# Kernel optimization log

Measured on AMD Instinct MI355X. Metric: run time of the kernel, lower is better.

The kernel has to match this reference:

```python
import jax, jax.numpy as jnp
import numpy as np

N = 50000        # nodes
E = 800000       # edges (before self-loops)
IN = 128         # in_dim
H = 2            # heads
C1 = 64          # hidden_dim (per head)
D1 = H * C1      # conv1 concat output = 128
OUT = 64         # out_dim
C2 = 2 * OUT     # conv2 per-head channels = 128 (concat=False -> mean over heads)
NEG = 0.2        # GATv2 leaky_relu negative slope
EPS = 1e-5       # BatchNorm eps


def setup_inputs() -> dict:
    key = jax.random.key(0)
    ks = jax.random.split(key, 14)
    s = 0.05
    inp = {
        "x": jax.random.normal(ks[0], (N, IN), jnp.float32),
        "edge_index": jax.random.randint(ks[1], (2, E), 0, N, dtype=jnp.int32),
        # conv1 (GATv2: lin_l for source, lin_r for target, att vector per head)
        "W_l1": jax.random.normal(ks[2], (IN, D1), jnp.float32) * s,
        "b_l1": jnp.zeros((D1,), jnp.float32),
        "W_r1": jax.random.normal(ks[3], (IN, D1), jnp.float32) * s,
        "b_r1": jnp.zeros((D1,), jnp.float32),
        "att1": jax.random.normal(ks[4], (H, C1), jnp.float32) * s,
        "bias1": jnp.zeros((D1,), jnp.float32),
        # batch_norm1 (affine)
        "gamma1": jnp.ones((D1,), jnp.float32),
        "beta1": jnp.zeros((D1,), jnp.float32),
        # conv2
        "W_l2": jax.random.normal(ks[5], (D1, H * C2), jnp.float32) * s,
        "b_l2": jnp.zeros((H * C2,), jnp.float32),
        "W_r2": jax.random.normal(ks[6], (D1, H * C2), jnp.float32) * s,
        "b_r2": jnp.zeros((H * C2,), jnp.float32),
        "att2": jax.random.normal(ks[7], (H, C2), jnp.float32) * s,
        "bias2": jnp.zeros((C2,), jnp.float32),
    }
    return inp


def gatv2_layer(x, src, dst, W_l, b_l, W_r, b_r, att, bias, concat):
    Hh, Cc = att.shape
    x_l = (x @ W_l + b_l).reshape(N, Hh, Cc)   # source transform
    x_r = (x @ W_r + b_r).reshape(N, Hh, Cc)   # target transform
    # per-edge GATv2 score: att . leaky_relu(x_l[j] + x_r[i])
    e = jax.nn.leaky_relu(x_l[src] + x_r[dst], NEG)      # [E', H, C]
    logit = jnp.einsum("ehc,hc->eh", e, att)              # [E', H]
    # segment softmax over incoming edges of each target node
    m = jax.ops.segment_max(logit, dst, num_segments=N)   # [N, H]
    ex = jnp.exp(logit - m[dst])
    den = jax.ops.segment_sum(ex, dst, num_segments=N)    # [N, H]
    alpha = ex / den[dst]                                  # [E', H]
    out = jax.ops.segment_sum(x_l[src] * alpha[:, :, None], dst, num_segments=N)
    out = out.reshape(N, Hh * Cc) if concat else out.mean(axis=1)
    return out + bias


def batchnorm(x, gamma=None, beta=None):
    mu = x.mean(axis=0)
    var = x.var(axis=0)  # biased variance, as used by BN for normalization
    xn = (x - mu) * jax.lax.rsqrt(var + EPS)
    if gamma is not None:
        xn = xn * gamma + beta
    return xn


def reference(x, edge_index, W_l1, b_l1, W_r1, b_r1, att1, bias1, gamma1, beta1,
              W_l2, b_l2, W_r2, b_r2, att2, bias2):
    loops = jnp.arange(N, dtype=edge_index.dtype)
    src = jnp.concatenate([edge_index[0], loops])  # add self-loops (PyG default)
    dst = jnp.concatenate([edge_index[1], loops])
    h = gatv2_layer(x, src, dst, W_l1, b_l1, W_r1, b_r1, att1, bias1, True)
    h = jax.nn.relu(batchnorm(h, gamma1, beta1))
    o = gatv2_layer(h, src, dst, W_l2, b_l2, W_r2, b_r2, att2, bias2, False)
    mu_part = batchnorm(o[:, :OUT])                      # affine=False
    return jnp.concatenate([mu_part, jax.nn.softplus(o[:, OUT:])], axis=1)
```

## Files before the change

### kernel.cpp

```cpp
#include <hip/hip_runtime.h>
#include <hip/hip_bf16.h>
#include <math.h>

#define NNODES 50000
#define NEDGES 800000
#define EPTOT  (NEDGES + NNODES)
#define NEG_SLOPE 0.2f
#define BN_EPS 1e-5f
#define LOG2E 1.44269504088896f
#define ESLOT 64

#define PB_SC  3321
#define PB_W1  (PB_SC + 128)
#define PB_W2  (PB_W1 + 256)

typedef __hip_bfloat16 bf16;
typedef __attribute__((ext_vector_type(8))) short short8;
typedef __attribute__((ext_vector_type(4))) float f32x4;
typedef __attribute__((ext_vector_type(2))) float f32x2;

__device__ __forceinline__ unsigned short f2us(float f){
    return (unsigned short)(__bfloat16_as_ushort(__float2bfloat16(f)));
}
__device__ __forceinline__ f32x2 unpk(unsigned int w){
    union { unsigned int u; float f; } lo, hi;
    lo.u = w << 16; hi.u = w & 0xffff0000u;
    f32x2 r; r.x = lo.f; r.y = hi.f; return r;
}
__device__ __forceinline__ f32x2 pkmax(f32x2 a, f32x2 b){
#if __has_builtin(__builtin_elementwise_max)
    return __builtin_elementwise_max(a, b);
#else
    f32x2 r; r.x = fmaxf(a.x, b.x); r.y = fmaxf(a.y, b.y); return r;
#endif
}
__device__ __forceinline__ unsigned int pack2(float a, float b){
    return (unsigned int)f2us(a) | ((unsigned int)f2us(b) << 16);
}

template<int CTRL>
__device__ __forceinline__ float dppadd(float v){
    int p = __builtin_amdgcn_update_dpp(0, __float_as_int(v), CTRL, 0xf, 0xf, true);
    return v + __int_as_float(p);
}
template<int G>
__device__ __forceinline__ float group_sum(float v){
    if constexpr (G == 16){
        v = dppadd<0x121>(v);
        v = dppadd<0x122>(v);
        v = dppadd<0x124>(v);
        v = dppadd<0x128>(v);
    } else {
        v = dppadd<0xB1>(v);
        v = dppadd<0x4E>(v);
        v += __shfl_xor(v, 4, 64);
    }
    return v;
}


__global__ __launch_bounds__(256) void misc_prep(
    const int* __restrict__ ei, int* __restrict__ cnt, int* __restrict__ esrc,
    const float* __restrict__ Wl1, const float* __restrict__ Wr1,
    const float* __restrict__ bl1, const float* __restrict__ br1,
    bf16* __restrict__ WT1, float* __restrict__ bc1,
    const float* __restrict__ Wl2, const float* __restrict__ Wr2,
    const float* __restrict__ bl2, const float* __restrict__ br2,
    bf16* __restrict__ WT2, float* __restrict__ bc2)
{
    int b = blockIdx.x;
    if (b < PB_SC){
        int e = b * 256 + threadIdx.x;
        if (e < EPTOT){
            int s, d;
            if (e < NEDGES){ s = ei[e]; d = ei[NEDGES + e]; } else { s = d = e - NEDGES; }
            int pos = atomicAdd(&cnt[d], 1);
            if (pos < ESLOT) esrc[(d << 6) + pos] = s;
        }
    } else if (b < PB_W1){
        int i = (b - PB_SC) * 256 + threadIdx.x;
        int r = i >> 7, k = i & 127;
        const float* W = (r < 128) ? Wl1 : Wr1;
        int c = (r < 128) ? r : r - 128;
        WT1[i] = __float2bfloat16(W[k * 128 + c]);
        if (k == 0) bc1[r] = (r < 128) ? bl1[c] : br1[c];
    } else {
        int i = (b - PB_W1) * 256 + threadIdx.x;
        int r = i >> 7, k = i & 127;
        const float* W = (r < 256) ? Wl2 : Wr2;
        int c = (r < 256) ? r : r - 256;
        WT2[i] = __float2bfloat16(W[k * 256 + c]);
        if (k == 0) bc2[r] = (r < 256) ? bl2[c] : br2[c];
    }
}


template<int DTOT, bool F32A, int NT>
__global__ __launch_bounds__(128) void mfma_gemm(
    const void* __restrict__ A, const bf16* __restrict__ WT,
    const float* __restrict__ biascat,
    bf16* __restrict__ xl, bf16* __restrict__ xr)
{
    int wave = threadIdx.x >> 6;
    int lane = threadIdx.x & 63;
    int quad = lane >> 4;
    int l16  = lane & 15;
    int m0 = blockIdx.x * 128 + wave * 64;
    const short* Ap = (const short*)A;
    const float* Af = (const float*)A;
    const short* Bp = (const short*)WT;

    short8 af[4][4];
    #pragma unroll
    for (int k = 0; k < 4; ++k)
        #pragma unroll
        for (int mt = 0; mt < 4; ++mt){
            int m = m0 + mt * 16 + l16;
            m = (m < NNODES) ? m : (NNODES - 1);
            if (F32A){
                float4 v0 = *(const float4*)(Af + (size_t)m * 128 + k * 32 + quad * 8);
                float4 v1 = *(const float4*)(Af + (size_t)m * 128 + k * 32 + quad * 8 + 4);
                unsigned int* u = (unsigned int*)&af[k][mt];
                u[0] = pack2(v0.x, v0.y); u[1] = pack2(v0.z, v0.w);
                u[2] = pack2(v1.x, v1.y); u[3] = pack2(v1.z, v1.w);
            } else {
                af[k][mt] = *(const short8*)(Ap + (size_t)m * 128 + k * 32 + quad * 8);
            }
        }

    for (int t = 0; t < NT; ++t){
        int n0 = (blockIdx.y * NT + t) * 64;
        f32x4 acc[4][4] = {};
        #pragma unroll
        for (int k = 0; k < 4; ++k){
            short8 bfr[4];
            #pragma unroll
            for (int nt = 0; nt < 4; ++nt){
                int n = n0 + nt * 16 + l16;
                bfr[nt] = *(const short8*)(Bp + (size_t)n * 128 + k * 32 + quad * 8);
            }
            #pragma unroll
            for (int mt = 0; mt < 4; ++mt)
                #pragma unroll
                for (int nt = 0; nt < 4; ++nt)
                    acc[mt][nt] = __builtin_amdgcn_mfma_f32_16x16x32_bf16(af[k][mt], bfr[nt], acc[mt][nt], 0, 0, 0);
        }
        #pragma unroll
        for (int nt = 0; nt < 4; ++nt){
            int n = n0 + nt * 16 + l16;
            float bi = biascat[n];
            bf16* outp = (n < DTOT) ? xl : xr;
            int c = (n < DTOT) ? n : n - DTOT;
            #pragma unroll
            for (int mt = 0; mt < 4; ++mt)
                #pragma unroll
                for (int r = 0; r < 4; ++r){
                    int m = m0 + mt * 16 + quad * 4 + r;
                    if (m < NNODES)
                        outp[(size_t)m * DTOT + c] = __float2bfloat16(acc[mt][nt][r] + bi);
                }
        }
    }
}


template<int C, bool MEAN>
__global__ __launch_bounds__(128) void gat_aggregate(
    const bf16* __restrict__ xl, const bf16* __restrict__ xr,
    const float* __restrict__ att, const int* __restrict__ cnt,
    const int* __restrict__ esrc, void* __restrict__ outv,
    const float* __restrict__ bias2)
{
    constexpr int G  = C / 8;
    constexpr int E  = 64 / G;
    constexpr int HC = 2 * C;
    __shared__ float tmp[HC];
    int n    = blockIdx.x;
    int lane = threadIdx.x & 63;
    int head = threadIdx.x >> 6;
    int g    = lane / G;
    int cl   = lane % G;
    int rowoff = head * (C * 2) + cl * 16;
    const char* xlp = (const char*)xl;

    int srcAll = esrc[(n << 6) + lane];
    int cc = cnt[n];
    int c = (cc < ESLOT) ? cc : ESLOT;
    uint4 xw = *(const uint4*)((const char*)xr + (unsigned)(n * (HC * 2) + rowoff));
    f32x2 xr0 = unpk(xw.x), xr1 = unpk(xw.y), xr2v = unpk(xw.z), xr3 = unpk(xw.w);
    const float* ap = att + head * C + cl * 8;
    f32x2 av0 = {ap[0] * LOG2E, ap[1] * LOG2E};
    f32x2 av1 = {ap[2] * LOG2E, ap[3] * LOG2E};
    f32x2 av2 = {ap[4] * LOG2E, ap[5] * LOG2E};
    f32x2 av3 = {ap[6] * LOG2E, ap[7] * LOG2E};

    float den = 0.f;
    f32x2 a0 = {0.f,0.f}, a1 = {0.f,0.f}, a2 = {0.f,0.f}, a3 = {0.f,0.f};

    int ia0 = g, ib0 = E + g;
    int sa = __shfl(srcAll, (ia0 < c) ? ia0 : (c - 1), 64);
    int sb = __shfl(srcAll, (ib0 < c) ? ib0 : (c - 1), 64);

    int p = 0;
    for (; p + E < c; p += 2 * E){
        uint4 wa = *(const uint4*)(xlp + ((unsigned)sa * (unsigned)(HC * 2) + rowoff));
        uint4 wb = *(const uint4*)(xlp + ((unsigned)sb * (unsigned)(HC * 2) + rowoff));
        float mkb = (p + E + g < c) ? 0.f : -1e30f;

        int pn = p + 2 * E;
        int ian = pn + g, ibn = pn + E + g;
        int sa_n = __shfl(srcAll, (ian < c) ? ian : (c - 1), 64);
        int sb_n = __shfl(srcAll, (ibn < c) ? ibn : (c - 1), 64);

        f32x2 xa0 = unpk(wa.x), xa1 = unpk(wa.y), xa2 = unpk(wa.z), xa3 = unpk(wa.w);
        f32x2 xb0 = unpk(wb.x), xb1 = unpk(wb.y), xb2 = unpk(wb.z), xb3 = unpk(wb.w);

        f32x2 ua0 = xa0 + xr0, ua1 = xa1 + xr1, ua2 = xa2 + xr2v, ua3 = xa3 + xr3;
        f32x2 ub0 = xb0 + xr0, ub1 = xb1 + xr1, ub2 = xb2 + xr2v, ub3 = xb3 + xr3;

        f32x2 ppa = pkmax(ua0, ua0 * NEG_SLOPE) * av0;
        ppa += pkmax(ua1, ua1 * NEG_SLOPE) * av1;
        ppa += pkmax(ua2, ua2 * NEG_SLOPE) * av2;
        ppa += pkmax(ua3, ua3 * NEG_SLOPE) * av3;
        f32x2 ppb = pkmax(ub0, ub0 * NEG_SLOPE) * av0;
        ppb += pkmax(ub1, ub1 * NEG_SLOPE) * av1;
        ppb += pkmax(ub2, ub2 * NEG_SLOPE) * av2;
        ppb += pkmax(ub3, ub3 * NEG_SLOPE) * av3;
        float parta = group_sum<G>(ppa.x + ppa.y);
        float partb = group_sum<G>(ppb.x + ppb.y);
        float exa = exp2f(parta);
        float exb = exp2f(partb + mkb);
        den += exa + exb;
        f32x2 ea = {exa, exa}, eb = {exb, exb};
        a0 += ea * xa0; a1 += ea * xa1; a2 += ea * xa2; a3 += ea * xa3;
        a0 += eb * xb0; a1 += eb * xb1; a2 += eb * xb2; a3 += eb * xb3;
        sa = sa_n; sb = sb_n;
    }
    if (p < c){
        float mka = (p + g < c) ? 0.f : -1e30f;
        uint4 wa = *(const uint4*)(xlp + ((unsigned)sa * (unsigned)(HC * 2) + rowoff));

        f32x2 xa0 = unpk(wa.x), xa1 = unpk(wa.y), xa2 = unpk(wa.z), xa3 = unpk(wa.w);
        f32x2 ua0 = xa0 + xr0, ua1 = xa1 + xr1, ua2 = xa2 + xr2v, ua3 = xa3 + xr3;

        f32x2 ppa = pkmax(ua0, ua0 * NEG_SLOPE) * av0;
        ppa += pkmax(ua1, ua1 * NEG_SLOPE) * av1;
        ppa += pkmax(ua2, ua2 * NEG_SLOPE) * av2;
        ppa += pkmax(ua3, ua3 * NEG_SLOPE) * av3;
        float parta = group_sum<G>(ppa.x + ppa.y);
        float exa = exp2f(parta + mka);
        den += exa;
        f32x2 ea = {exa, exa};
        a0 += ea * xa0; a1 += ea * xa1; a2 += ea * xa2; a3 += ea * xa3;
    }

    #pragma unroll
    for (int mask = G; mask < 64; mask <<= 1){
        den  += __shfl_xor(den, mask, 64);
        a0.x += __shfl_xor(a0.x, mask, 64); a0.y += __shfl_xor(a0.y, mask, 64);
        a1.x += __shfl_xor(a1.x, mask, 64); a1.y += __shfl_xor(a1.y, mask, 64);
        a2.x += __shfl_xor(a2.x, mask, 64); a2.y += __shfl_xor(a2.y, mask, 64);
        a3.x += __shfl_xor(a3.x, mask, 64); a3.y += __shfl_xor(a3.y, mask, 64);
    }
    float inv = 1.f / den;

    if (!MEAN){
        if (g == 0){
            uint4 o;
            o.x = pack2(a0.x * inv, a0.y * inv);
            o.y = pack2(a1.x * inv, a1.y * inv);
            o.z = pack2(a2.x * inv, a2.y * inv);
            o.w = pack2(a3.x * inv, a3.y * inv);
            *(uint4*)((char*)outv + (size_t)n * (HC * 2) + rowoff) = o;
        }
    } else {
        if (g == 0){
            float* tp = tmp + head * C + cl * 8;
            tp[0] = a0.x * inv; tp[1] = a0.y * inv;
            tp[2] = a1.x * inv; tp[3] = a1.y * inv;
            tp[4] = a2.x * inv; tp[5] = a2.y * inv;
            tp[6] = a3.x * inv; tp[7] = a3.y * inv;
        }
        __syncthreads();
        if (head == 0 && g == 0){
            float* outp = (float*)outv + (size_t)n * C;
            #pragma unroll
            for (int v = 0; v < 8; ++v){
                int c2 = cl * 8 + v;
                outp[c2] = 0.5f * (tmp[c2] + tmp[C + c2]) + bias2[c2];
            }
        }
    }
}


__global__ void bn_stats_bf16(const unsigned int* __restrict__ x, float* __restrict__ sums){
    __shared__ float ls[1024];
    int t = threadIdx.x;
    int c2 = t & 63;
    int rg = t >> 6;
    float s0 = 0.f, q0 = 0.f, s1 = 0.f, q1 = 0.f;
    for (int r = blockIdx.x * 4 + rg; r < NNODES; r += gridDim.x * 4){
        f32x2 v = unpk(x[(size_t)r * 64 + c2]);
        s0 += v.x; q0 += v.x * v.x;
        s1 += v.y; q1 += v.y * v.y;
    }
    ls[t] = s0; ls[256 + t] = q0; ls[512 + t] = s1; ls[768 + t] = q1;
    __syncthreads();
    if (rg == 0){
        for (int g = 1; g < 4; ++g){
            s0 += ls[g * 64 + c2];       q0 += ls[256 + g * 64 + c2];
            s1 += ls[512 + g * 64 + c2]; q1 += ls[768 + g * 64 + c2];
        }
        atomicAdd(&sums[2 * c2], s0);
        atomicAdd(&sums[128 + 2 * c2], q0);
        atomicAdd(&sums[2 * c2 + 1], s1);
        atomicAdd(&sums[128 + 2 * c2 + 1], q1);
    }
}

__global__ void bn_stats_o2(const float* __restrict__ x, float* __restrict__ sums){
    __shared__ float ls[512];
    int t = threadIdx.x;
    int col = t & 63;
    int rg  = t >> 6;
    float s = 0.f, q = 0.f;
    for (int r = blockIdx.x * 4 + rg; r < NNODES; r += gridDim.x * 4){
        float v = x[(size_t)r * 128 + col];
        s += v; q += v * v;
    }
    ls[t] = s; ls[256 + t] = q;
    __syncthreads();
    if (rg == 0){
        for (int g = 1; g < 4; ++g){ s += ls[g * 64 + col]; q += ls[256 + g * 64 + col]; }
        atomicAdd(&sums[col], s);
        atomicAdd(&sums[64 + col], q);
    }
}

__global__ void bn_apply_relu(const unsigned int* __restrict__ o1, const float* __restrict__ sums,
                              const float* __restrict__ gamma, const float* __restrict__ beta,
                              unsigned int* __restrict__ h){
    int i = blockIdx.x * blockDim.x + threadIdx.x;
    if (i >= NNODES * 64) return;
    int c2 = i & 63;
    int c0 = 2 * c2, c1 = c0 + 1;
    const float inv_n = 1.f / (float)NNODES;
    float mu0 = sums[c0] * inv_n;
    float sc0 = gamma[c0] * rsqrtf(sums[128 + c0] * inv_n - mu0 * mu0 + BN_EPS);
    float sh0 = beta[c0] - mu0 * sc0;
    float mu1 = sums[c1] * inv_n;
    float sc1 = gamma[c1] * rsqrtf(sums[128 + c1] * inv_n - mu1 * mu1 + BN_EPS);
    float sh1 = beta[c1] - mu1 * sc1;
    f32x2 v = unpk(o1[i]);
    float v0 = v.x * sc0 + sh0;
    float v1 = v.y * sc1 + sh1;
    h[i] = pack2(v0 > 0.f ? v0 : 0.f, v1 > 0.f ? v1 : 0.f);
}

__global__ void final_out(const float* __restrict__ o2, const float* __restrict__ sums,
                          float* __restrict__ out){
    int i = blockIdx.x * blockDim.x + threadIdx.x;
    if (i >= NNODES * 32) return;
    float4 v = *(const float4*)(o2 + (size_t)i * 4);
    int c = (i * 4) & 127;
    const float* vp = (const float*)&v;
    float4 r;
    float* rp = (float*)&r;
    if (c < 64){
        const float inv_n = 1.f / (float)NNODES;
        #pragma unroll
        for (int k = 0; k < 4; ++k){
            float mu = sums[c + k] * inv_n;
            float rsig = rsqrtf(sums[64 + c + k] * inv_n - mu * mu + BN_EPS);
            rp[k] = (vp[k] - mu) * rsig;
        }
    } else {
        #pragma unroll
        for (int k = 0; k < 4; ++k){
            float x = vp[k];
            rp[k] = (x > 20.f) ? x : log1pf(__expf(x));
        }
    }
    *(float4*)(out + (size_t)i * 4) = r;
}


extern "C" void kernel_launch(void* const* d_in, const int* in_sizes, int n_in,
                              void* d_out, int out_size, void* d_ws, size_t ws_size,
                              hipStream_t stream) {
    const float* x     = (const float*)d_in[0];
    const int*   ei    = (const int*)d_in[1];
    const float* W_l1  = (const float*)d_in[2];
    const float* b_l1  = (const float*)d_in[3];
    const float* W_r1  = (const float*)d_in[4];
    const float* b_r1  = (const float*)d_in[5];
    const float* att1  = (const float*)d_in[6];
    const float* gamma1 = (const float*)d_in[8];
    const float* beta1  = (const float*)d_in[9];
    const float* W_l2  = (const float*)d_in[10];
    const float* b_l2  = (const float*)d_in[11];
    const float* W_r2  = (const float*)d_in[12];
    const float* b_r2  = (const float*)d_in[13];
    const float* att2  = (const float*)d_in[14];
    const float* bias2 = (const float*)d_in[15];
    float* out = (float*)d_out;

    char* w = (char*)d_ws;
    size_t off = 0;
    auto alloc = [&](size_t bytes) -> void* {
        void* p = w + off;
        off += (bytes + 255) & ~(size_t)255;
        return p;
    };
    const size_t NF  = (size_t)NNODES * 128 * 4;
    bf16*  xl1   = (bf16*) alloc(NF / 2);
    bf16*  xr1   = (bf16*) alloc(NF / 2);
    bf16*  xl2   = (bf16*) alloc(NF);
    bf16*  xr2   = (bf16*) alloc(NF);
    bf16*  hbuf  = (bf16*) alloc(NF / 2);
    unsigned int* o1 = (unsigned int*)alloc(NF / 2);
    float* o2    = (float*)alloc(NF);
    bf16*  WT1   = (bf16*) alloc(256 * 128 * 2);
    bf16*  WT2   = (bf16*) alloc(512 * 128 * 2);
    float* bc1   = (float*)alloc(256 * 4);
    float* bc2   = (float*)alloc(512 * 4);
    int*   cnt    = (int*)  alloc((size_t)NNODES * 4);
    int*   esrc   = (int*)  alloc((size_t)NNODES * ESLOT * 4);
    float* bnsums = (float*)alloc(384 * 4);
    float* bn1s = bnsums;
    float* bn2s = bnsums + 256;

    hipMemsetAsync(cnt, 0, (size_t)NNODES * 4, stream);
    hipMemsetAsync(bnsums, 0, 384 * 4, stream);

    misc_prep<<<PB_W2, 256, 0, stream>>>(ei, cnt, esrc,
                                         W_l1, W_r1, b_l1, b_r1, WT1, bc1,
                                         W_l2, W_r2, b_l2, b_r2, WT2, bc2);

    mfma_gemm<128, true, 2><<<dim3(392, 2), 128, 0, stream>>>(x, WT1, bc1, xl1, xr1);
    gat_aggregate<64, false><<<NNODES, 128, 0, stream>>>(xl1, xr1, att1, cnt, esrc, o1, bias2);

    bn_stats_bf16<<<512, 256, 0, stream>>>(o1, bn1s);
    bn_apply_relu<<<(NNODES * 64 + 255) / 256, 256, 0, stream>>>(o1, bn1s, gamma1, beta1, (unsigned int*)hbuf);

    mfma_gemm<256, false, 2><<<dim3(392, 4), 128, 0, stream>>>(hbuf, WT2, bc2, xl2, xr2);
    gat_aggregate<128, true><<<NNODES, 128, 0, stream>>>(xl2, xr2, att2, cnt, esrc, o2, bias2);

    bn_stats_o2<<<512, 256, 0, stream>>>(o2, bn2s);
    final_out<<<(NNODES * 32 + 255) / 256, 256, 0, stream>>>(o2, bn2s, out);
}
```

Measured before the change: 413.3 us.

## Fuse BN1+ReLU into second GEMM load and map one node per wave

The separate batchnorm-apply+ReLU kernel and its intermediate buffer are removed. The second GEMM now reads the raw layer-1 output and applies scale/shift/ReLU while loading its A operand. The aggregation kernel is restructured so each 64-lane wave handles one node with both heads at once, 4 nodes per 256-thread block. The head-mean is then done with a lane shuffle instead of shared memory and __syncthreads. This cuts one launch plus a full read/write pass and reduces per-block overhead, at the cost of redundant BN-parameter computation in every GEMM block and fewer lanes per edge in the aggregation.

```diff
diff --git a/kernel.cpp b/kernel.cpp
--- a/kernel.cpp
+++ b/kernel.cpp
@@ -95,38 +95,64 @@
 }
 
 
-template<int DTOT, bool F32A, int NT>
+template<int DTOT, int AMODE, int NT>
 __global__ __launch_bounds__(128) void mfma_gemm(
     const void* __restrict__ A, const bf16* __restrict__ WT,
     const float* __restrict__ biascat,
-    bf16* __restrict__ xl, bf16* __restrict__ xr)
+    bf16* __restrict__ xl, bf16* __restrict__ xr,
+    const float* __restrict__ bns, const float* __restrict__ gamma,
+    const float* __restrict__ beta)
 {
     int wave = threadIdx.x >> 6;
     int lane = threadIdx.x & 63;
     int quad = lane >> 4;
     int l16  = lane & 15;
     int m0 = blockIdx.x * 128 + wave * 64;
-    const short* Ap = (const short*)A;
     const float* Af = (const float*)A;
+    const unsigned int* Ao = (const unsigned int*)A;
     const short* Bp = (const short*)WT;
 
     short8 af[4][4];
     #pragma unroll
-    for (int k = 0; k < 4; ++k)
+    for (int k = 0; k < 4; ++k){
+        float sc[8], sh[8];
+        if (AMODE == 2){
+            const float inv_n = 1.f / (float)NNODES;
+            int cb = k * 32 + quad * 8;
+            #pragma unroll
+            for (int j = 0; j < 8; ++j){
+                float mu = bns[cb + j] * inv_n;
+                float s  = gamma[cb + j] * rsqrtf(bns[128 + cb + j] * inv_n - mu * mu + BN_EPS);
+                sc[j] = s; sh[j] = beta[cb + j] - mu * s;
+            }
+        }
         #pragma unroll
         for (int mt = 0; mt < 4; ++mt){
             int m = m0 + mt * 16 + l16;
             m = (m < NNODES) ? m : (NNODES - 1);
-            if (F32A){
+            if (AMODE == 1){
                 float4 v0 = *(const float4*)(Af + (size_t)m * 128 + k * 32 + quad * 8);
                 float4 v1 = *(const float4*)(Af + (size_t)m * 128 + k * 32 + quad * 8 + 4);
                 unsigned int* u = (unsigned int*)&af[k][mt];
                 u[0] = pack2(v0.x, v0.y); u[1] = pack2(v0.z, v0.w);
                 u[2] = pack2(v1.x, v1.y); u[3] = pack2(v1.z, v1.w);
             } else {
-                af[k][mt] = *(const short8*)(Ap + (size_t)m * 128 + k * 32 + quad * 8);
+                uint4 w = *(const uint4*)(Ao + (size_t)m * 64 + k * 16 + quad * 4);
+                f32x2 v0 = unpk(w.x), v1 = unpk(w.y), v2 = unpk(w.z), v3 = unpk(w.w);
+                float f0 = v0.x * sc[0] + sh[0], f1 = v0.y * sc[1] + sh[1];
+                float f2 = v1.x * sc[2] + sh[2], f3 = v1.y * sc[3] + sh[3];
+                float f4 = v2.x * sc[4] + sh[4], f5 = v2.y * sc[5] + sh[5];
+                float f6 = v3.x * sc[6] + sh[6], f7 = v3.y * sc[7] + sh[7];
+                f0 = f0 > 0.f ? f0 : 0.f; f1 = f1 > 0.f ? f1 : 0.f;
+                f2 = f2 > 0.f ? f2 : 0.f; f3 = f3 > 0.f ? f3 : 0.f;
+                f4 = f4 > 0.f ? f4 : 0.f; f5 = f5 > 0.f ? f5 : 0.f;
+                f6 = f6 > 0.f ? f6 : 0.f; f7 = f7 > 0.f ? f7 : 0.f;
+                unsigned int* u = (unsigned int*)&af[k][mt];
+                u[0] = pack2(f0, f1); u[1] = pack2(f2, f3);
+                u[2] = pack2(f4, f5); u[3] = pack2(f6, f7);
             }
         }
+    }
 
     for (int t = 0; t < NT; ++t){
         int n0 = (blockIdx.y * NT + t) * 64;
@@ -165,50 +191,56 @@
 
 
 template<int C, bool MEAN>
-__global__ __launch_bounds__(128) void gat_aggregate(
+__global__ __launch_bounds__(256) void gat_aggregate(
     const bf16* __restrict__ xl, const bf16* __restrict__ xr,
     const float* __restrict__ att, const int* __restrict__ cnt,
     const int* __restrict__ esrc, void* __restrict__ outv,
     const float* __restrict__ bias2)
 {
-    constexpr int G  = C / 8;
-    constexpr int E  = 64 / G;
-    constexpr int HC = 2 * C;
-    __shared__ float tmp[HC];
-    int n    = blockIdx.x;
+    constexpr int GH  = C / 8;
+    constexpr int LPE = 2 * GH;
+    constexpr int EL  = 64 / LPE;
+    constexpr int RB  = 4 * C;
     int lane = threadIdx.x & 63;
-    int head = threadIdx.x >> 6;
-    int g    = lane / G;
-    int cl   = lane % G;
-    int rowoff = head * (C * 2) + cl * 16;
+    int wave = threadIdx.x >> 6;
+    int n    = blockIdx.x * 4 + wave;
+    int el   = lane / LPE;
+    int h    = (lane / GH) & 1;
+    int cl   = lane % GH;
+    int rowoff = h * (C * 2) + cl * 16;
     const char* xlp = (const char*)xl;
 
     int srcAll = esrc[(n << 6) + lane];
     int cc = cnt[n];
     int c = (cc < ESLOT) ? cc : ESLOT;
-    uint4 xw = *(const uint4*)((const char*)xr + (unsigned)(n * (HC * 2) + rowoff));
+    uint4 xw = *(const uint4*)((const char*)xr + (unsigned)n * RB + rowoff);
     f32x2 xr0 = unpk(xw.x), xr1 = unpk(xw.y), xr2v = unpk(xw.z), xr3 = unpk(xw.w);
-    const float* ap = att + head * C + cl * 8;
+    const float* ap = att + h * C + cl * 8;
     f32x2 av0 = {ap[0] * LOG2E, ap[1] * LOG2E};
     f32x2 av1 = {ap[2] * LOG2E, ap[3] * LOG2E};
     f32x2 av2 = {ap[4] * LOG2E, ap[5] * LOG2E};
     f32x2 av3 = {ap[6] * LOG2E, ap[7] * LOG2E};
+    float b2r[8];
+    if (MEAN){
+        #pragma unroll
+        for (int v = 0; v < 8; ++v) b2r[v] = bias2[cl * 8 + v];
+    }
 
     float den = 0.f;
     f32x2 a0 = {0.f,0.f}, a1 = {0.f,0.f}, a2 = {0.f,0.f}, a3 = {0.f,0.f};
 
-    int ia0 = g, ib0 = E + g;
+    int ia0 = el, ib0 = EL + el;
     int sa = __shfl(srcAll, (ia0 < c) ? ia0 : (c - 1), 64);
     int sb = __shfl(srcAll, (ib0 < c) ? ib0 : (c - 1), 64);
 
     int p = 0;
-    for (; p + E < c; p += 2 * E){
-        uint4 wa = *(const uint4*)(xlp + ((unsigned)sa * (unsigned)(HC * 2) + rowoff));
-        uint4 wb = *(const uint4*)(xlp + ((unsigned)sb * (unsigned)(HC * 2) + rowoff));
-        float mkb = (p + E + g < c) ? 0.f : -1e30f;
-
-        int pn = p + 2 * E;
-        int ian = pn + g, ibn = pn + E + g;
+    for (; p + EL < c; p += 2 * EL){
+        uint4 wa = *(const uint4*)(xlp + ((unsigned)sa * (unsigned)RB + rowoff));
+        uint4 wb = *(const uint4*)(xlp + ((unsigned)sb * (unsigned)RB + rowoff));
+        float mkb = (p + EL + el < c) ? 0.f : -1e30f;
+
+        int pn = p + 2 * EL;
+        int ian = pn + el, ibn = pn + EL + el;
         int sa_n = __shfl(srcAll, (ian < c) ? ian : (c - 1), 64);
         int sb_n = __shfl(srcAll, (ibn < c) ? ibn : (c - 1), 64);
 
@@ -226,8 +258,8 @@
         ppb += pkmax(ub1, ub1 * NEG_SLOPE) * av1;
         ppb += pkmax(ub2, ub2 * NEG_SLOPE) * av2;
         ppb += pkmax(ub3, ub3 * NEG_SLOPE) * av3;
-        float parta = group_sum<G>(ppa.x + ppa.y);
-        float partb = group_sum<G>(ppb.x + ppb.y);
+        float parta = group_sum<GH>(ppa.x + ppa.y);
+        float partb = group_sum<GH>(ppb.x + ppb.y);
         float exa = exp2f(parta);
         float exb = exp2f(partb + mkb);
         den += exa + exb;
@@ -237,8 +269,8 @@
         sa = sa_n; sb = sb_n;
     }
     if (p < c){
-        float mka = (p + g < c) ? 0.f : -1e30f;
-        uint4 wa = *(const uint4*)(xlp + ((unsigned)sa * (unsigned)(HC * 2) + rowoff));
+        float mka = (p + el < c) ? 0.f : -1e30f;
+        uint4 wa = *(const uint4*)(xlp + ((unsigned)sa * (unsigned)RB + rowoff));
 
         f32x2 xa0 = unpk(wa.x), xa1 = unpk(wa.y), xa2 = unpk(wa.z), xa3 = unpk(wa.w);
         f32x2 ua0 = xa0 + xr0, ua1 = xa1 + xr1, ua2 = xa2 + xr2v, ua3 = xa3 + xr3;
@@ -247,7 +279,7 @@
         ppa += pkmax(ua1, ua1 * NEG_SLOPE) * av1;
         ppa += pkmax(ua2, ua2 * NEG_SLOPE) * av2;
         ppa += pkmax(ua3, ua3 * NEG_SLOPE) * av3;
-        float parta = group_sum<G>(ppa.x + ppa.y);
+        float parta = group_sum<GH>(ppa.x + ppa.y);
         float exa = exp2f(parta + mka);
         den += exa;
         f32x2 ea = {exa, exa};
@@ -255,7 +287,7 @@
     }
 
     #pragma unroll
-    for (int mask = G; mask < 64; mask <<= 1){
+    for (int mask = LPE; mask < 64; mask <<= 1){
         den  += __shfl_xor(den, mask, 64);
         a0.x += __shfl_xor(a0.x, mask, 64); a0.y += __shfl_xor(a0.y, mask, 64);
         a1.x += __shfl_xor(a1.x, mask, 64); a1.y += __shfl_xor(a1.y, mask, 64);
@@ -265,30 +297,31 @@
     float inv = 1.f / den;
 
     if (!MEAN){
-        if (g == 0){
+        if (el == 0){
             uint4 o;
             o.x = pack2(a0.x * inv, a0.y * inv);
             o.y = pack2(a1.x * inv, a1.y * inv);
             o.z = pack2(a2.x * inv, a2.y * inv);
             o.w = pack2(a3.x * inv, a3.y * inv);
-            *(uint4*)((char*)outv + (size_t)n * (HC * 2) + rowoff) = o;
+            *(uint4*)((char*)outv + (size_t)n * RB + rowoff) = o;
         }
     } else {
-        if (g == 0){
-            float* tp = tmp + head * C + cl * 8;
-            tp[0] = a0.x * inv; tp[1] = a0.y * inv;
-            tp[2] = a1.x * inv; tp[3] = a1.y * inv;
-            tp[4] = a2.x * inv; tp[5] = a2.y * inv;
-            tp[6] = a3.x * inv; tp[7] = a3.y * inv;
-        }
-        __syncthreads();
-        if (head == 0 && g == 0){
-            float* outp = (float*)outv + (size_t)n * C;
-            #pragma unroll
-            for (int v = 0; v < 8; ++v){
-                int c2 = cl * 8 + v;
-                outp[c2] = 0.5f * (tmp[c2] + tmp[C + c2]) + bias2[c2];
-            }
+        float v0 = a0.x * inv, v1 = a0.y * inv, v2 = a1.x * inv, v3 = a1.y * inv;
+        float v4 = a2.x * inv, v5 = a2.y * inv, v6 = a3.x * inv, v7 = a3.y * inv;
+        v0 = 0.5f * (v0 + __shfl_xor(v0, 16, 64)) + b2r[0];
+        v1 = 0.5f * (v1 + __shfl_xor(v1, 16, 64)) + b2r[1];
+        v2 = 0.5f * (v2 + __shfl_xor(v2, 16, 64)) + b2r[2];
+        v3 = 0.5f * (v3 + __shfl_xor(v3, 16, 64)) + b2r[3];
+        v4 = 0.5f * (v4 + __shfl_xor(v4, 16, 64)) + b2r[4];
+        v5 = 0.5f * (v5 + __shfl_xor(v5, 16, 64)) + b2r[5];
+        v6 = 0.5f * (v6 + __shfl_xor(v6, 16, 64)) + b2r[6];
+        v7 = 0.5f * (v7 + __shfl_xor(v7, 16, 64)) + b2r[7];
+        if (el == 0 && h == 0){
+            float* outp = (float*)outv + (size_t)n * C + cl * 8;
+            float4 w0 = {v0, v1, v2, v3};
+            float4 w1 = {v4, v5, v6, v7};
+            *(float4*)(outp) = w0;
+            *(float4*)(outp + 4) = w1;
         }
     }
 }
@@ -336,26 +369,6 @@
         atomicAdd(&sums[col], s);
         atomicAdd(&sums[64 + col], q);
     }
-}
-
-__global__ void bn_apply_relu(const unsigned int* __restrict__ o1, const float* __restrict__ sums,
-                              const float* __restrict__ gamma, const float* __restrict__ beta,
-                              unsigned int* __restrict__ h){
-    int i = blockIdx.x * blockDim.x + threadIdx.x;
-    if (i >= NNODES * 64) return;
-    int c2 = i & 63;
-    int c0 = 2 * c2, c1 = c0 + 1;
-    const float inv_n = 1.f / (float)NNODES;
-    float mu0 = sums[c0] * inv_n;
-    float sc0 = gamma[c0] * rsqrtf(sums[128 + c0] * inv_n - mu0 * mu0 + BN_EPS);
-    float sh0 = beta[c0] - mu0 * sc0;
-    float mu1 = sums[c1] * inv_n;
-    float sc1 = gamma[c1] * rsqrtf(sums[128 + c1] * inv_n - mu1 * mu1 + BN_EPS);
-    float sh1 = beta[c1] - mu1 * sc1;
-    f32x2 v = unpk(o1[i]);
-    float v0 = v.x * sc0 + sh0;
-    float v1 = v.y * sc1 + sh1;
-    h[i] = pack2(v0 > 0.f ? v0 : 0.f, v1 > 0.f ? v1 : 0.f);
 }
 
 __global__ void final_out(const float* __restrict__ o2, const float* __restrict__ sums,
@@ -418,7 +431,6 @@
     bf16*  xr1   = (bf16*) alloc(NF / 2);
     bf16*  xl2   = (bf16*) alloc(NF);
     bf16*  xr2   = (bf16*) alloc(NF);
-    bf16*  hbuf  = (bf16*) alloc(NF / 2);
     unsigned int* o1 = (unsigned int*)alloc(NF / 2);
     float* o2    = (float*)alloc(NF);
     bf16*  WT1   = (bf16*) alloc(256 * 128 * 2);
@@ -438,14 +450,15 @@
                                          W_l1, W_r1, b_l1, b_r1, WT1, bc1,
                                          W_l2, W_r2, b_l2, b_r2, WT2, bc2);
 
-    mfma_gemm<128, true, 2><<<dim3(392, 2), 128, 0, stream>>>(x, WT1, bc1, xl1, xr1);
-    gat_aggregate<64, false><<<NNODES, 128, 0, stream>>>(xl1, xr1, att1, cnt, esrc, o1, bias2);
+    mfma_gemm<128, 1, 2><<<dim3(392, 2), 128, 0, stream>>>(x, WT1, bc1, xl1, xr1,
+                                                           nullptr, nullptr, nullptr);
+    gat_aggregate<64, false><<<NNODES / 4, 256, 0, stream>>>(xl1, xr1, att1, cnt, esrc, o1, bias2);
 
     bn_stats_bf16<<<512, 256, 0, stream>>>(o1, bn1s);
-    bn_apply_relu<<<(NNODES * 64 + 255) / 256, 256, 0, stream>>>(o1, bn1s, gamma1, beta1, (unsigned int*)hbuf);
-
-    mfma_gemm<256, false, 2><<<dim3(392, 4), 128, 0, stream>>>(hbuf, WT2, bc2, xl2, xr2);
-    gat_aggregate<128, true><<<NNODES, 128, 0, stream>>>(xl2, xr2, att2, cnt, esrc, o2, bias2);
+
+    mfma_gemm<256, 2, 2><<<dim3(392, 4), 128, 0, stream>>>(o1, WT2, bc2, xl2, xr2,
+                                                           bn1s, gamma1, beta1);
+    gat_aggregate<128, true><<<NNODES / 4, 256, 0, stream>>>(xl2, xr2, att2, cnt, esrc, o2, bias2);
 
     bn_stats_o2<<<512, 256, 0, stream>>>(o2, bn2s);
     final_out<<<(NNODES * 32 + 255) / 256, 256, 0, stream>>>(o2, bn2s, out);
```

New measurement: 401.6 us. 2.8% less time.
